# Performance work log

Measured on AMD Instinct MI355X. Metric: run time of the kernel, lower is better.

Reference implementation:

```python
import jax, jax.numpy as jnp
import numpy as np

NUM_HEADS = 12


def setup_inputs() -> dict:
    key = jax.random.key(0)
    ks = jax.random.split(key, 6)
    B, H, W, C = 8, 32, 32, 768
    hd = C // NUM_HEADS
    n = lambda k, shp, sc: jax.random.normal(k, shp, dtype=jnp.float32) * sc
    return {
        "x": n(ks[0], (B, H, W, C), 1.0),
        "qkv_w": n(ks[1], (3 * C, C), 0.02),
        "qkv_b": jnp.zeros((3 * C,), jnp.float32),
        "proj_w": n(ks[2], (C, C), 0.02),
        "proj_b": jnp.zeros((C,), jnp.float32),
        "rel_pos_h": n(ks[3], (2 * H - 1, hd), 0.02),
        "rel_pos_w": n(ks[4], (2 * W - 1, hd), 0.02),
    }


def reference(x, qkv_w, qkv_b, proj_w, proj_b, rel_pos_h, rel_pos_w):
    B, H, W, C = x.shape
    nH = NUM_HEADS
    hd = C // nH
    scale = hd ** -0.5
    # qkv projection (torch Linear convention: y = x @ W.T + b)
    qkv = x.reshape(B, H * W, C) @ qkv_w.T + qkv_b              # (B, HW, 3C)
    qkv = qkv.reshape(B, H * W, 3, nH, hd).transpose(2, 0, 3, 1, 4)
    qkv = qkv.reshape(3, B * nH, H * W, hd)
    q, k, v = qkv[0], qkv[1], qkv[2]
    attn = jnp.einsum('bqd,bkd->bqk', q * scale, k)             # (B*nH, HW, HW)
    # decomposed relative position bias (q_size == k_size, so no interpolation)
    coords_h = jnp.arange(H)[:, None] - jnp.arange(H)[None, :] + (H - 1)
    coords_w = jnp.arange(W)[:, None] - jnp.arange(W)[None, :] + (W - 1)
    Rh = rel_pos_h[coords_h]                                    # (H, H, hd)
    Rw = rel_pos_w[coords_w]                                    # (W, W, hd)
    r_q = q.reshape(B * nH, H, W, hd)
    rel_h = jnp.einsum('bhwc,hkc->bhwk', r_q, Rh)               # (B*nH, H, W, H)
    rel_w = jnp.einsum('bhwc,wkc->bhwk', r_q, Rw)               # (B*nH, H, W, W)
    attn = (attn.reshape(B * nH, H, W, H, W)
            + rel_h[..., :, None] + rel_w[..., None, :]).reshape(B * nH, H * W, H * W)
    attn = jax.nn.softmax(attn, axis=-1)
    out = attn @ v                                              # (B*nH, HW, hd)
    out = out.reshape(B, nH, H, W, hd).transpose(0, 2, 3, 1, 4).reshape(B, H, W, C)
    return out @ proj_w.T + proj_b
```

## Files before the change

### kernel.cpp

```cpp
#include <hip/hip_runtime.h>

using u16 = unsigned short;
using u32 = unsigned int;
typedef __attribute__((ext_vector_type(8))) short bf16x8;
typedef __attribute__((ext_vector_type(4))) float f32x4;

__device__ __forceinline__ float bf2f(u32 h) {
  union { u32 u; float f; } c; c.u = h << 16; return c.f;
}
__device__ __forceinline__ u16 f2bf(float f) {
  union { float f; u32 u; } c; c.f = f;
  u32 u = c.u;
  u32 r = (u + 0x7FFFu + ((u >> 16) & 1u)) >> 16;
  return (u16)r;
}

#define GLD16(gsrc, ldst)                                                      \
  __builtin_amdgcn_global_load_lds(                                            \
      (const __attribute__((address_space(1))) unsigned int*)(gsrc),           \
      (__attribute__((address_space(3))) unsigned int*)(ldst), 16, 0, 0)

__device__ __forceinline__ int kappa(int ss) {
  return (ss & 0x23) | ((ss & 0x10) >> 2) | ((ss & 0x0C) << 1);
}

__device__ __forceinline__ bf16x8 onehot8(int c) {
  union { u32 w[4]; bf16x8 v; } u;
  u32 hv = (c & 1) ? 0x3F800000u : 0x3F80u;
#pragma unroll
  for (int k = 0; k < 4; ++k) u.w[k] = ((c >> 1) == k) ? hv : 0u;
  return u.v;
}

__global__ void prep_kernel(const float* __restrict__ x, const float* __restrict__ qw,
                            const float* __restrict__ pw, const float* __restrict__ rph,
                            const float* __restrict__ rpw, u16* __restrict__ xb,
                            u16* __restrict__ qwb, u16* __restrict__ pwb,
                            u16* __restrict__ tbl) {
  int i = blockIdx.x * 256 + threadIdx.x;
  const float* src;
  u16* dst;
  int j;
  if (i < 1572864) { src = x; dst = xb; j = i; }
  else if (i < 2015232) { src = qw; dst = qwb; j = i - 1572864; }
  else if (i < 2162688) { src = pw; dst = pwb; j = i - 2015232; }
  else {
    int b = (i - 2162688) * 4;
    ushort4 o;
#pragma unroll
    for (int k = 0; k < 4; ++k) {
      int idx = b + k, row = idx >> 6, d = idx & 63;
      float v = 0.f;
      if (row < 63) v = rph[row * 64 + d];
      else if (row >= 64 && row < 127) v = rpw[(row - 64) * 64 + d];
      ((u16*)&o)[k] = f2bf(v * 8.0f);
    }
    *(ushort4*)&tbl[b] = o;
    return;
  }
  float4 v = *(const float4*)(src + j * 4);
  ushort4 o;
  o.x = f2bf(v.x); o.y = f2bf(v.y); o.z = f2bf(v.z); o.w = f2bf(v.w);
  *(ushort4*)(dst + j * 4) = o;
}

__global__ __launch_bounds__(256, 2) void pgemm_kernel(
    const u16* __restrict__ A, const u16* __restrict__ tbl, u16* __restrict__ Q2) {
  __shared__ u16 Bs[128 * 64];
  const int tid = threadIdx.x;
  const int lane = tid & 63, wave = tid >> 6;
  const int lr = lane & 15, lg = lane >> 4;
  const int m0 = blockIdx.x * 256;
  const int wm = (wave >> 1) * 64, wn = (wave & 1) * 64;

#pragma unroll
  for (int i = 0; i < 4; ++i) {
    int c = tid + i * 256;
    int row = c >> 3, pp = c & 7;
    int pl = pp ^ (row & 7);
    GLD16(tbl + row * 64 + pl * 8, &Bs[c * 8]);
  }
  __syncthreads();

  bf16x8 b[4][2];
#pragma unroll
  for (int n = 0; n < 4; ++n) {
    int row = wn + n * 16 + lr;
#pragma unroll
    for (int kf = 0; kf < 2; ++kf)
      b[n][kf] = *(const bf16x8*)&Bs[(row * 64 + kf * 32 + lg * 8) ^ ((row & 7) << 3)];
  }

#pragma unroll
  for (int tt = 0; tt < 2; ++tt) {
    bf16x8 a[4][2];
#pragma unroll
    for (int m = 0; m < 4; ++m) {
      int g = m0 + tt * 128 + wm + m * 16 + lr;
#pragma unroll
      for (int kf = 0; kf < 2; ++kf)
        a[m][kf] = *(const bf16x8*)(A + (size_t)g * 128 + kf * 32 + lg * 8);
    }
    f32x4 acc[4][4] = {};
#pragma unroll
    for (int kf = 0; kf < 2; ++kf)
#pragma unroll
      for (int m = 0; m < 4; ++m)
#pragma unroll
        for (int n = 0; n < 4; ++n)
          acc[m][n] = __builtin_amdgcn_mfma_f32_16x16x32_bf16(a[m][kf], b[n][kf], acc[m][n], 0, 0, 0);

#pragma unroll
    for (int m = 0; m < 4; ++m)
#pragma unroll
      for (int n = 0; n < 4; ++n) {
        const int col = wn + n * 16 + lr;
#pragma unroll
        for (int r = 0; r < 4; ++r) {
          const int g = m0 + tt * 128 + wm + m * 16 + lg * 4 + r;
          const int s = g & 1023;
          const int hq = s >> 5, w = s & 31;
          u16 hv = f2bf(acc[m][n][r]);
          if (col < 64) {
            int kh = hq + 31 - col;
            if ((unsigned)kh < 32u) Q2[(size_t)g * 128 + 96 + kh] = hv;
          } else {
            int kw = w + 95 - col;
            if ((unsigned)kw < 32u) Q2[(size_t)g * 128 + 64 + kw] = hv;
          }
        }
      }
  }
}

template <int MODE>
__global__ __launch_bounds__(512, 2) void gemm128(
    const u16* __restrict__ A, const u16* __restrict__ B,
    const float* __restrict__ bias, u16* __restrict__ oq, u16* __restrict__ ok,
    u16* __restrict__ ovt, float* __restrict__ ofp) {
  __shared__ u16 As[2][128 * 64];
  __shared__ u16 Bs[2][128 * 64];
  const int tid = threadIdx.x;
  const int lane = tid & 63, wave = tid >> 6;
  const int lr = lane & 15, lg = lane >> 4;

  const int nbx = (MODE == 0) ? 18 : 6;
  const int nwg = nbx * 64;
  int id = blockIdx.y * nbx + blockIdx.x;
  int nid = (id & 7) * (nwg >> 3) + (id >> 3);
  const int m0 = (nid / nbx) * 128, n0 = (nid % nbx) * 128;
  const int wm = (wave >> 2) * 64, wn = (wave & 3) * 32;

  f32x4 acc[4][2] = {};

  int aoff[4][2], boff[2][2];
#pragma unroll
  for (int m = 0; m < 4; ++m) {
    int row = wm + m * 16 + lr;
#pragma unroll
    for (int kf = 0; kf < 2; ++kf)
      aoff[m][kf] = (row * 64 + kf * 32 + lg * 8) ^ ((row & 7) << 3);
  }
#pragma unroll
  for (int n = 0; n < 2; ++n) {
    int row = wn + n * 16 + lr;
#pragma unroll
    for (int kf = 0; kf < 2; ++kf)
      boff[n][kf] = (row * 64 + kf * 32 + lg * 8) ^ ((row & 7) << 3);
  }

  const u16* ap[2];
  const u16* bp[2];
#pragma unroll
  for (int i = 0; i < 2; ++i) {
    int c = tid + i * 512;
    int row = c >> 3, pp = c & 7;
    int pl = pp ^ (row & 7);
    if constexpr (MODE == 0) {
      ap[i] = A + (size_t)(m0 + row) * 768 + pl * 8;
    } else {
      int g = m0 + row;
      ap[i] = A + ((size_t)((g >> 10) * 12) << 16) + (g & 1023) * 64 + pl * 8;
    }
    bp[i] = B + (size_t)(n0 + row) * 768 + pl * 8;
  }
  constexpr int dA = (MODE == 0) ? 64 : 65536;

  auto stage = [&](int bi) {
#pragma unroll
    for (int i = 0; i < 2; ++i) {
      int c = tid + i * 512;
      GLD16(ap[i], &As[bi][c * 8]);
      GLD16(bp[i], &Bs[bi][c * 8]);
      ap[i] += dA;
      bp[i] += 64;
    }
  };

  stage(0);
#pragma unroll 1
  for (int t = 0; t < 12; ++t) {
    const int cur = t & 1;
    if (t < 11) {
      stage(cur ^ 1);
      asm volatile("s_waitcnt vmcnt(4)" ::: "memory");
    } else {
      asm volatile("s_waitcnt vmcnt(0)" ::: "memory");
    }
    __builtin_amdgcn_sched_barrier(0);
    __builtin_amdgcn_s_barrier();
    __builtin_amdgcn_sched_barrier(0);

    bf16x8 a[4][2], b[2][2];
#pragma unroll
    for (int m = 0; m < 4; ++m)
#pragma unroll
      for (int kf = 0; kf < 2; ++kf)
        a[m][kf] = *(const bf16x8*)&As[cur][aoff[m][kf]];
#pragma unroll
    for (int n = 0; n < 2; ++n)
#pragma unroll
      for (int kf = 0; kf < 2; ++kf)
        b[n][kf] = *(const bf16x8*)&Bs[cur][boff[n][kf]];
    __builtin_amdgcn_s_setprio(1);
#pragma unroll
    for (int kf = 0; kf < 2; ++kf)
#pragma unroll
      for (int m = 0; m < 4; ++m)
#pragma unroll
        for (int n = 0; n < 2; ++n)
          acc[m][n] = __builtin_amdgcn_mfma_f32_16x16x32_bf16(a[m][kf], b[n][kf], acc[m][n], 0, 0, 0);
    __builtin_amdgcn_s_setprio(0);

    __builtin_amdgcn_sched_barrier(0);
    __builtin_amdgcn_s_barrier();
    __builtin_amdgcn_sched_barrier(0);
  }

#pragma unroll
  for (int m = 0; m < 4; ++m) {
    const int grow0 = m0 + wm + m * 16 + lg * 4;
#pragma unroll
    for (int n = 0; n < 2; ++n) {
      const int gcol = n0 + wn + n * 16 + lr;
      const float bv = bias[gcol];
      if constexpr (MODE == 0) {
        int which = (gcol >= 1536) ? 2 : (gcol >= 768 ? 1 : 0);
        int rem = gcol - which * 768;
        int bh = (grow0 >> 10) * 12 + (rem >> 6);
        if (which == 2) {
          int s0 = grow0 & 1023;
          int colb = (s0 & ~63) | kappa(s0 & 63);
          ushort4 pk;
          pk.x = f2bf(acc[m][n][0] + bv);
          pk.y = f2bf(acc[m][n][1] + bv);
          pk.z = f2bf(acc[m][n][2] + bv);
          pk.w = f2bf(acc[m][n][3] + bv);
          *(ushort4*)&ovt[((size_t)bh << 16) + (size_t)(rem & 63) * 1024 + colb] = pk;
        } else if (which == 0) {
#pragma unroll
          for (int r = 0; r < 4; ++r) {
            int s = (grow0 & 1023) + r;
            oq[((size_t)bh << 17) + s * 128 + (rem & 63)] =
                f2bf((acc[m][n][r] + bv) * 0.18033688f);
          }
        } else {
#pragma unroll
          for (int r = 0; r < 4; ++r) {
            int s = (grow0 & 1023) + r;
            ok[((size_t)bh << 16) + s * 64 + (rem & 63)] = f2bf(acc[m][n][r] + bv);
          }
        }
      } else {
#pragma unroll
        for (int r = 0; r < 4; ++r)
          ofp[(size_t)(grow0 + r) * 768 + gcol] = acc[m][n][r] + bv;
      }
    }
  }
}

__global__ __launch_bounds__(256, 2) void attn_kernel(
    const u16* __restrict__ qb, const u16* __restrict__ kb,
    const u16* __restrict__ vtb, u16* __restrict__ ao) {
  __shared__ u16 Ks[2][4096];
  __shared__ u16 Vs[2][4096];

  const int tid = threadIdx.x;
  const int lane = tid & 63, wave = tid >> 6;
  const int lr = lane & 15, lg = lane >> 4;
  const int bh = blockIdx.x;
  const int q0 = blockIdx.y * 128 + wave * 32;
  const size_t hb2 = (size_t)bh << 17;
  const size_t hbv = (size_t)bh << 16;

  bf16x8 qf[2][4];
#pragma unroll
  for (int m = 0; m < 2; ++m)
#pragma unroll
    for (int kf = 0; kf < 4; ++kf)
      qf[m][kf] = *(const bf16x8*)(qb + hb2 + (size_t)(q0 + m * 16 + lr) * 128 + kf * 32 + lg * 8);

  f32x4 sacW[2][2] = {};
#pragma unroll
  for (int h = 0; h < 2; ++h) {
    bf16x8 kwf = onehot8(h * 16 + lr - lg * 8);
#pragma unroll
    for (int m = 0; m < 2; ++m)
      sacW[m][h] = __builtin_amdgcn_mfma_f32_16x16x32_bf16(kwf, qf[m][2], sacW[m][h], 0, 0, 0);
  }

  float lsum[2] = {};
  f32x4 acco[2][4] = {};

  const u16* kp[2];
  const u16* vp[2];
#pragma unroll
  for (int i = 0; i < 2; ++i) {
    int c = tid + i * 256;
    int row = c >> 3, pp = c & 7;
    int pl = pp ^ (row & 7);
    kp[i] = kb + hbv + (size_t)row * 64 + pl * 8;
    vp[i] = vtb + hbv + (size_t)row * 1024 + pl * 8;
  }

  auto stage = [&](int bi) {
#pragma unroll
    for (int i = 0; i < 2; ++i) {
      int c = tid + i * 256;
      GLD16(kp[i], &Ks[bi][c * 8]);
      GLD16(vp[i], &Vs[bi][c * 8]);
      kp[i] += 4096;
      vp[i] += 64;
    }
  };

  stage(0);

#pragma unroll 1
  for (int t = 0; t < 16; ++t) {
    const int cur = t & 1;
    if (t < 15) {
      stage(cur ^ 1);
      asm volatile("s_waitcnt vmcnt(4)" ::: "memory");
    } else {
      asm volatile("s_waitcnt vmcnt(0)" ::: "memory");
    }
    __builtin_amdgcn_sched_barrier(0);
    __builtin_amdgcn_s_barrier();
    __builtin_amdgcn_sched_barrier(0);

    bf16x8 khf[2];
#pragma unroll
    for (int h = 0; h < 2; ++h) khf[h] = onehot8(2 * t + h - lg * 8);

    f32x4 sac[2][4];
#pragma unroll
    for (int m = 0; m < 2; ++m)
#pragma unroll
      for (int f = 0; f < 4; ++f) sac[m][f] = sacW[m][f & 1];
    __builtin_amdgcn_s_setprio(1);
#pragma unroll
    for (int kf = 0; kf < 2; ++kf) {
#pragma unroll
      for (int f = 0; f < 4; ++f) {
        int row = f * 16 + lr;
        bf16x8 kv = *(const bf16x8*)&Ks[cur][(row * 64 + kf * 32 + lg * 8) ^ ((row & 7) << 3)];
#pragma unroll
        for (int m = 0; m < 2; ++m)
          sac[m][f] = __builtin_amdgcn_mfma_f32_16x16x32_bf16(kv, qf[m][kf], sac[m][f], 0, 0, 0);
      }
    }
#pragma unroll
    for (int f = 0; f < 4; ++f)
#pragma unroll
      for (int m = 0; m < 2; ++m)
        sac[m][f] = __builtin_amdgcn_mfma_f32_16x16x32_bf16(khf[f >> 1], qf[m][3], sac[m][f], 0, 0, 0);
    __builtin_amdgcn_s_setprio(0);

    bf16x8 paf[2][2];
#pragma unroll
    for (int m = 0; m < 2; ++m) {
      union { u32 w[4]; bf16x8 v; } wa, wb;
#pragma unroll
      for (int f = 0; f < 4; ++f) {
        float p0 = __builtin_amdgcn_exp2f(sac[m][f][0]);
        float p1 = __builtin_amdgcn_exp2f(sac[m][f][1]);
        float p2 = __builtin_amdgcn_exp2f(sac[m][f][2]);
        float p3 = __builtin_amdgcn_exp2f(sac[m][f][3]);
        lsum[m] += (p0 + p1) + (p2 + p3);
        u32 w0, w1;
        asm("v_cvt_pk_bf16_f32 %0, %1, %2" : "=v"(w0) : "v"(p0), "v"(p1));
        asm("v_cvt_pk_bf16_f32 %0, %1, %2" : "=v"(w1) : "v"(p2), "v"(p3));
        if (f < 2) { wa.w[f * 2] = w0; wa.w[f * 2 + 1] = w1; }
        else       { wb.w[(f - 2) * 2] = w0; wb.w[(f - 2) * 2 + 1] = w1; }
      }
      paf[m][0] = wa.v;
      paf[m][1] = wb.v;
    }

    __builtin_amdgcn_s_setprio(1);
#pragma unroll
    for (int kf = 0; kf < 2; ++kf) {
#pragma unroll
      for (int fd = 0; fd < 4; ++fd) {
        int drow = fd * 16 + lr;
        bf16x8 vv = *(const bf16x8*)&Vs[cur][(drow * 64 + kf * 32 + lg * 8) ^ ((drow & 7) << 3)];
#pragma unroll
        for (int m = 0; m < 2; ++m)
          acco[m][fd] = __builtin_amdgcn_mfma_f32_16x16x32_bf16(paf[m][kf], vv, acco[m][fd], 0, 0, 0);
      }
    }
    __builtin_amdgcn_s_setprio(0);

    __builtin_amdgcn_sched_barrier(0);
    __builtin_amdgcn_s_barrier();
    __builtin_amdgcn_sched_barrier(0);
  }

#pragma unroll
  for (int m = 0; m < 2; ++m) {
    float s = lsum[m];
    s += __shfl_xor(s, 16);
    s += __shfl_xor(s, 32);
    float inv = 1.0f / s;
#pragma unroll
    for (int r = 0; r < 4; ++r) {
      int src = (lane & 48) + ((lane & 48) >> 2) + r;
      float invr = __shfl(inv, src);
      int gq = q0 + m * 16 + lg * 4 + r;
#pragma unroll
      for (int fd = 0; fd < 4; ++fd)
        ao[hbv + (size_t)gq * 64 + fd * 16 + lr] = f2bf(acco[m][fd][r] * invr);
    }
  }
}

extern "C" void kernel_launch(void* const* d_in, const int* in_sizes, int n_in,
                              void* d_out, int out_size, void* d_ws, size_t ws_size,
                              hipStream_t stream) {
  const float* x = (const float*)d_in[0];
  const float* qkv_w = (const float*)d_in[1];
  const float* qkv_b = (const float*)d_in[2];
  const float* proj_w = (const float*)d_in[3];
  const float* proj_b = (const float*)d_in[4];
  const float* rel_pos_h = (const float*)d_in[5];
  const float* rel_pos_w = (const float*)d_in[6];
  float* out = (float*)d_out;

  char* ws = (char*)d_ws;
  u16* x_bf = (u16*)(ws + 0);
  u16* qkvw_bf = (u16*)(ws + 12582912);
  u16* projw_bf = (u16*)(ws + 16121856);
  u16* qbuf2 = (u16*)(ws + 17301504);
  u16* kbuf = (u16*)(ws + 42467328);
  u16* vtbuf = (u16*)(ws + 55050240);
  u16* tbl = (u16*)(ws + 67633152);
  u16* aobuf = x_bf;

  prep_kernel<<<8456, 256, 0, stream>>>(x, qkv_w, proj_w, rel_pos_h, rel_pos_w,
                                        x_bf, qkvw_bf, projw_bf, tbl);

  gemm128<0><<<dim3(18, 64), 512, 0, stream>>>(x_bf, qkvw_bf, qkv_b, qbuf2, kbuf, vtbuf, nullptr);

  pgemm_kernel<<<384, 256, 0, stream>>>(qbuf2, tbl, qbuf2);

  attn_kernel<<<dim3(96, 8), 256, 0, stream>>>(qbuf2, kbuf, vtbuf, aobuf);

  gemm128<1><<<dim3(6, 64), 512, 0, stream>>>(aobuf, projw_bf, proj_b, nullptr, nullptr, nullptr, out);
}
```

Baseline: 120.7 us.

## Use 256x256-tile pipelined GEMM for the QKV projection

Adds a gemm256 kernel that computes a 256x256 output tile per workgroup, split into four 128x128 quadrants, with double-buffered LDS staging interleaved across quadrant MFMA phases. The kernel is used for the QKV projection in place of the 128x128 gemm128, cutting the grid from 1152 to 288 workgroups and doubling operand reuse per LDS load. In exchange it uses 128KB LDS per block and heavy register pressure, and 288 blocks may underfill the GPU's 256 CUs (a partial second wave).

```diff
diff --git a/kernel.cpp b/kernel.cpp
--- a/kernel.cpp
+++ b/kernel.cpp
@@ -131,6 +131,202 @@
         }
       }
   }
+}
+
+template <int MODE>
+__global__ __launch_bounds__(512, 2) void gemm256(
+    const u16* __restrict__ A, const u16* __restrict__ B,
+    const float* __restrict__ bias, u16* __restrict__ oq, u16* __restrict__ ok,
+    u16* __restrict__ ovt, float* __restrict__ ofp) {
+  __shared__ u16 As[2][16384];
+  __shared__ u16 Bs[2][16384];
+  const int tid = threadIdx.x;
+  const int lane = tid & 63, wave = tid >> 6;
+  const int lr = lane & 15, lg = lane >> 4;
+
+  const int nbx = (MODE == 0) ? 9 : 3;
+  const int nwg = nbx * 32;
+  int id = blockIdx.y * nbx + blockIdx.x;
+  int nid = (id & 7) * (nwg >> 3) + (id >> 3);
+  const int m0 = (nid / nbx) * 256, n0 = (nid % nbx) * 256;
+  const int wm64 = (wave >> 2) * 64, wn32 = (wave & 3) * 32;
+
+  f32x4 acc[8][4] = {};
+
+  int aoff[4][2], boff[2][2];
+#pragma unroll
+  for (int m = 0; m < 4; ++m) {
+    int row = wm64 + m * 16 + lr;
+#pragma unroll
+    for (int kf = 0; kf < 2; ++kf)
+      aoff[m][kf] = (row * 64 + kf * 32 + lg * 8) ^ ((row & 7) << 3);
+  }
+#pragma unroll
+  for (int n = 0; n < 2; ++n) {
+    int row = wn32 + n * 16 + lr;
+#pragma unroll
+    for (int kf = 0; kf < 2; ++kf)
+      boff[n][kf] = (row * 64 + kf * 32 + lg * 8) ^ ((row & 7) << 3);
+  }
+
+  const u16* pA[2][2];
+  const u16* pB[2][2];
+#pragma unroll
+  for (int h = 0; h < 2; ++h)
+#pragma unroll
+    for (int i2 = 0; i2 < 2; ++i2) {
+      int c = tid + i2 * 512;
+      int row = c >> 3, pp = c & 7;
+      int pl = pp ^ (row & 7);
+      if constexpr (MODE == 0) {
+        pA[h][i2] = A + (size_t)(m0 + h * 128 + row) * 768 + pl * 8;
+      } else {
+        int g = m0 + h * 128 + row;
+        pA[h][i2] = A + ((size_t)((g >> 10) * 12) << 16) + (g & 1023) * 64 + pl * 8;
+      }
+      pB[h][i2] = B + (size_t)(n0 + h * 128 + row) * 768 + pl * 8;
+    }
+  constexpr int dA = (MODE == 0) ? 64 : 65536;
+
+  auto stageA = [&](int half, int slot) {
+    GLD16(pA[half][0], &As[slot][half * 8192 + tid * 8]);
+    GLD16(pA[half][1], &As[slot][half * 8192 + (tid + 512) * 8]);
+    pA[half][0] += dA;
+    pA[half][1] += dA;
+  };
+  auto stageB = [&](int half, int slot) {
+    GLD16(pB[half][0], &Bs[slot][half * 8192 + tid * 8]);
+    GLD16(pB[half][1], &Bs[slot][half * 8192 + (tid + 512) * 8]);
+    pB[half][0] += 64;
+    pB[half][1] += 64;
+  };
+
+  stageA(0, 0); stageA(1, 0); stageB(0, 0); stageB(1, 0);
+  stageA(0, 1); stageA(1, 1);
+  asm volatile("s_waitcnt vmcnt(4)" ::: "memory");
+  __builtin_amdgcn_sched_barrier(0);
+  __builtin_amdgcn_s_barrier();
+  __builtin_amdgcn_sched_barrier(0);
+
+  bf16x8 a[4][2], b0[2][2], b1[2][2];
+
+#pragma unroll 1
+  for (int i = 0; i < 6; ++i) {
+#pragma unroll
+    for (int j = 0; j < 8; ++j) {
+      const int tc = j >> 2;
+      const int q = j & 3;
+      const int mh = q >> 1, nh = q & 1;
+
+      if (q == 0) {
+#pragma unroll
+        for (int m = 0; m < 4; ++m)
+#pragma unroll
+          for (int kf = 0; kf < 2; ++kf)
+            a[m][kf] = *(const bf16x8*)&As[tc][aoff[m][kf]];
+#pragma unroll
+        for (int n = 0; n < 2; ++n)
+#pragma unroll
+          for (int kf = 0; kf < 2; ++kf)
+            b0[n][kf] = *(const bf16x8*)&Bs[tc][boff[n][kf]];
+      } else if (q == 1) {
+#pragma unroll
+        for (int n = 0; n < 2; ++n)
+#pragma unroll
+          for (int kf = 0; kf < 2; ++kf)
+            b1[n][kf] = *(const bf16x8*)&Bs[tc][8192 + boff[n][kf]];
+      } else if (q == 2) {
+#pragma unroll
+        for (int m = 0; m < 4; ++m)
+#pragma unroll
+          for (int kf = 0; kf < 2; ++kf)
+            a[m][kf] = *(const bf16x8*)&As[tc][8192 + aoff[m][kf]];
+      }
+
+      if (j == 0) stageB(0, 1);
+      else if (j == 1) stageB(1, 1);
+      else if (i < 5) {
+        if (j == 2) stageA(0, 0);
+        else if (j == 3) stageA(1, 0);
+        else if (j == 4) stageB(0, 0);
+        else if (j == 5) stageB(1, 0);
+        else if (j == 6) stageA(0, 1);
+        else stageA(1, 1);
+      }
+
+      __builtin_amdgcn_sched_barrier(0);
+      __builtin_amdgcn_s_barrier();
+      __builtin_amdgcn_sched_barrier(0);
+
+      __builtin_amdgcn_s_setprio(1);
+#pragma unroll
+      for (int kf = 0; kf < 2; ++kf)
+#pragma unroll
+        for (int m = 0; m < 4; ++m)
+#pragma unroll
+          for (int n = 0; n < 2; ++n)
+            acc[mh * 4 + m][nh * 2 + n] = __builtin_amdgcn_mfma_f32_16x16x32_bf16(
+                a[m][kf], (nh ? b1 : b0)[n][kf], acc[mh * 4 + m][nh * 2 + n], 0, 0, 0);
+      __builtin_amdgcn_s_setprio(0);
+      __builtin_amdgcn_sched_barrier(0);
+
+      if (j == 3) {
+        if (i < 5) asm volatile("s_waitcnt vmcnt(4)" ::: "memory");
+        else asm volatile("s_waitcnt vmcnt(0)" ::: "memory");
+      } else if (j == 7 && i < 5) {
+        asm volatile("s_waitcnt vmcnt(4)" ::: "memory");
+      }
+      __builtin_amdgcn_s_barrier();
+      __builtin_amdgcn_sched_barrier(0);
+    }
+  }
+
+#pragma unroll
+  for (int mh = 0; mh < 2; ++mh)
+#pragma unroll
+    for (int m = 0; m < 4; ++m) {
+      const int grow0 = m0 + mh * 128 + wm64 + m * 16 + lg * 4;
+#pragma unroll
+      for (int nh = 0; nh < 2; ++nh)
+#pragma unroll
+        for (int n = 0; n < 2; ++n) {
+          const int gcol = n0 + nh * 128 + wn32 + n * 16 + lr;
+          const float bv = bias[gcol];
+          f32x4 av = acc[mh * 4 + m][nh * 2 + n];
+          if constexpr (MODE == 0) {
+            int which = (gcol >= 1536) ? 2 : (gcol >= 768 ? 1 : 0);
+            int rem = gcol - which * 768;
+            int bh = (grow0 >> 10) * 12 + (rem >> 6);
+            if (which == 2) {
+              int s0 = grow0 & 1023;
+              int colb = (s0 & ~63) | kappa(s0 & 63);
+              ushort4 pk;
+              pk.x = f2bf(av[0] + bv);
+              pk.y = f2bf(av[1] + bv);
+              pk.z = f2bf(av[2] + bv);
+              pk.w = f2bf(av[3] + bv);
+              *(ushort4*)&ovt[((size_t)bh << 16) + (size_t)(rem & 63) * 1024 + colb] = pk;
+            } else if (which == 0) {
+#pragma unroll
+              for (int r = 0; r < 4; ++r) {
+                int s = (grow0 & 1023) + r;
+                oq[((size_t)bh << 17) + s * 128 + (rem & 63)] =
+                    f2bf((av[r] + bv) * 0.18033688f);
+              }
+            } else {
+#pragma unroll
+              for (int r = 0; r < 4; ++r) {
+                int s = (grow0 & 1023) + r;
+                ok[((size_t)bh << 16) + s * 64 + (rem & 63)] = f2bf(av[r] + bv);
+              }
+            }
+          } else {
+#pragma unroll
+            for (int r = 0; r < 4; ++r)
+              ofp[(size_t)(grow0 + r) * 768 + gcol] = av[r] + bv;
+          }
+        }
+    }
 }
 
 template <int MODE>
@@ -461,7 +657,7 @@
   prep_kernel<<<8456, 256, 0, stream>>>(x, qkv_w, proj_w, rel_pos_h, rel_pos_w,
                                         x_bf, qkvw_bf, projw_bf, tbl);
 
-  gemm128<0><<<dim3(18, 64), 512, 0, stream>>>(x_bf, qkvw_bf, qkv_b, qbuf2, kbuf, vtbuf, nullptr);
+  gemm256<0><<<dim3(9, 32), 512, 0, stream>>>(x_bf, qkvw_bf, qkv_b, qbuf2, kbuf, vtbuf, nullptr);
 
   pgemm_kernel<<<384, 256, 0, stream>>>(qbuf2, tbl, qbuf2);
 
```

Result: slower. 134.8 us (+11.6%).
